# Optimization experiments

Hardware: AMD Instinct MI355X
Metric: run time of the kernel (lower is better)

The kernel has to match this reference:

```python
import jax, jax.numpy as jnp
import numpy as np

B, L, E = 2, 8192, 1024
H, D = 16, 64          # num_heads, head_dim (E = H*D)
C = 256                # chunk_size
EPS = 1e-6
LN_EPS = 1e-5


def setup_inputs() -> dict:
    key = jax.random.key(0)
    ks = jax.random.split(key, 12)
    w = lambda k, shape: (jax.random.normal(k, shape, jnp.float32) * 0.02)
    return {
        "x": jax.random.normal(ks[0], (B, L, E), jnp.float32),
        "Wq": w(ks[1], (E, E)), "bq": jnp.zeros((E,), jnp.float32),
        "Wk": w(ks[2], (E, E)), "bk": jnp.zeros((E,), jnp.float32),
        "Wv": w(ks[3], (E, E)), "bv": jnp.zeros((E,), jnp.float32),
        "Wo": w(ks[4], (E, E)), "bo": jnp.zeros((E,), jnp.float32),
        "gamma": jnp.ones((E,), jnp.float32),
        "beta": jnp.zeros((E,), jnp.float32),
    }


def _split_heads(t):
    # [B, L, E] -> [B, H, L, D]
    return t.reshape(B, L, H, D).transpose(0, 2, 1, 3)


def _phi(x):
    # feature map: elu(x) + 1  (strictly positive)
    return jax.nn.elu(x) + 1.0


def _chunkwise_linear_attention(q, k, v):
    """Causal linear attention via chunkwise parallel scan.

    q, k, v: [B, H, L, D] (q, k already feature-mapped, positive).
    out[t] = q_t @ S_t / (q_t . z_t), S_t = sum_{s<=t} k_s v_s^T, z_t = sum_{s<=t} k_s.
    """
    N = L // C
    # [N, B, H, C, D]
    qc = q.reshape(B, H, N, C, D).transpose(2, 0, 1, 3, 4)
    kc = k.reshape(B, H, N, C, D).transpose(2, 0, 1, 3, 4)
    vc = v.reshape(B, H, N, C, D).transpose(2, 0, 1, 3, 4)
    mask = jnp.tril(jnp.ones((C, C), q.dtype))  # causal within chunk (inclusive)

    def step(carry, inp):
        S, z = carry                      # S: [B,H,D,D], z: [B,H,D]
        qi, ki, vi = inp                  # [B,H,C,D]
        scores = jnp.einsum("bhcd,bhed->bhce", qi, ki) * mask  # [B,H,C,C]
        num = jnp.einsum("bhcd,bhde->bhce", qi, S) \
            + jnp.einsum("bhce,bhed->bhcd", scores, vi)
        den = jnp.einsum("bhcd,bhd->bhc", qi, z) + scores.sum(-1)
        out = num / (den + EPS)[..., None]
        S = S + jnp.einsum("bhcd,bhce->bhde", ki, vi)
        z = z + ki.sum(axis=2)
        return (S, z), out

    S0 = jnp.zeros((B, H, D, D), q.dtype)
    z0 = jnp.zeros((B, H, D), q.dtype)
    _, outs = jax.lax.scan(step, (S0, z0), (qc, kc, vc))
    # [N,B,H,C,D] -> [B,H,L,D]
    return outs.transpose(1, 2, 0, 3, 4).reshape(B, H, L, D)


def _layer_norm(x, gamma, beta):
    mu = x.mean(-1, keepdims=True)
    var = ((x - mu) ** 2).mean(-1, keepdims=True)
    return gamma * (x - mu) * jax.lax.rsqrt(var + LN_EPS) + beta


def reference(x, Wq, bq, Wk, bk, Wv, bv, Wo, bo, gamma, beta):
    residual = x
    q = _phi(_split_heads(x @ Wq + bq))
    k = _phi(_split_heads(x @ Wk + bk))
    v = _split_heads(x @ Wv + bv)
    out = _chunkwise_linear_attention(q, k, v)      # [B,H,L,D]
    out = out.transpose(0, 2, 1, 3).reshape(B, L, E)
    out = out @ Wo + bo
    return _layer_norm(out + residual, gamma, beta)
```

## Files before the change

kernel.cpp:

```cpp
#include <hip/hip_runtime.h>
#include <stdint.h>

typedef __attribute__((ext_vector_type(8))) short bf16x8;
typedef __attribute__((ext_vector_type(4))) float f32x4;
typedef __attribute__((ext_vector_type(2))) unsigned int u32x2;
typedef unsigned short u16;
typedef unsigned int u32;

#define MFMA16(a, b, c) __builtin_amdgcn_mfma_f32_16x16x32_bf16((a), (b), (c), 0, 0, 0)

__device__ __forceinline__ u16 f2bf(float f) {
  union { float f; u32 u; } c; c.f = f;
  u32 u = c.u;
  return (u16)((u + 0x7FFFu + ((u >> 16) & 1u)) >> 16);
}

__device__ __forceinline__ float bf2f(u16 h) {
  union { u32 u; float f; } c;
  c.u = ((u32)h) << 16;
  return c.f;
}

__device__ __forceinline__ void gll16(const void* g, void* l) {
  __builtin_amdgcn_global_load_lds((__attribute__((address_space(1))) void*)(g),
                                   (__attribute__((address_space(3))) void*)(l),
                                   16, 0, 0);
}

__global__ __launch_bounds__(256) void cast_k(const float* __restrict__ x, u16* __restrict__ xb) {
  int idx = blockIdx.x * 256 + threadIdx.x;
#pragma unroll
  for (int it = 0; it < 4; it++) {
    size_t i = (size_t)idx + (size_t)it * 1048576;
    float4 v = ((const float4*)x)[i];
    u32x2 p;
    p.x = (u32)f2bf(v.x) | ((u32)f2bf(v.y) << 16);
    p.y = (u32)f2bf(v.z) | ((u32)f2bf(v.w) << 16);
    ((u32x2*)xb)[i] = p;
  }
}

__global__ __launch_bounds__(256) void wT_k(const float* __restrict__ Wq, const float* __restrict__ Wk,
                                            const float* __restrict__ Wv, const float* __restrict__ Wo,
                                            u16* __restrict__ wqkvT, u16* __restrict__ woT) {
  __shared__ float t[32][33];
  int which = blockIdx.z;
  const float* W = (which == 0) ? Wq : (which == 1) ? Wk : (which == 2) ? Wv : Wo;
  int k0 = blockIdx.y * 32, n0 = blockIdx.x * 32;
  int c = threadIdx.x & 31, r8 = threadIdx.x >> 5;
#pragma unroll
  for (int rr = 0; rr < 32; rr += 8)
    t[r8 + rr][c] = W[(size_t)(k0 + r8 + rr) * 1024 + n0 + c];
  __syncthreads();
  u16* outp = (which < 3) ? (wqkvT + (size_t)which * 1048576) : woT;
#pragma unroll
  for (int rr = 0; rr < 32; rr += 8)
    outp[(size_t)(n0 + r8 + rr) * 1024 + k0 + c] = f2bf(t[c][r8 + rr]);
}

template <int MODE>
__global__ __launch_bounds__(256, 2) void gemm_k(
    const u16* __restrict__ A, const u16* __restrict__ Bt,
    const float* __restrict__ b0, const float* __restrict__ b1, const float* __restrict__ b2,
    u16* __restrict__ q_o, u16* __restrict__ k_o, u16* __restrict__ vt_o,
    const u16* __restrict__ xres, u16* __restrict__ y_o) {
  __shared__ u16 As[2][4096];
  __shared__ u16 Bs[2][4096];
  const int tid = threadIdx.x;
  const int wave = tid >> 6, lane = tid & 63;
  const int quad = lane >> 4, l16 = lane & 15;
  const int wr = wave >> 1, wc = wave & 1;
  const int bm = blockIdx.x, bn = blockIdx.y;

  const int r_a = wave * 32 + (lane >> 2);
  const int c_a = (lane & 3) * 8;
  const size_t arow = (size_t)bm * 128;
  const size_t brow = (size_t)bn * 128;

  f32x4 zero = {0.f, 0.f, 0.f, 0.f};
  f32x4 acc[4][4];
#pragma unroll
  for (int i = 0; i < 4; i++)
#pragma unroll
    for (int j = 0; j < 4; j++) acc[i][j] = zero;

  for (int k0 = 0; k0 < 1024; k0 += 64) {
#pragma unroll
    for (int h = 0; h < 2; h++) {
      const int kk = k0 + h * 32;
#pragma unroll
      for (int jc = 0; jc < 2; jc++) {
        int r = r_a + jc * 16;
        int lo = wave * 1024 + jc * 512 + lane * 8;
        gll16(A + (arow + r) * 1024 + kk + c_a, &As[h][lo]);
        gll16(Bt + (brow + r) * 1024 + kk + c_a, &Bs[h][lo]);
      }
    }
    __syncthreads();
#pragma unroll
    for (int h = 0; h < 2; h++) {
      bf16x8 af[4], bf[4];
#pragma unroll
      for (int t = 0; t < 4; t++) af[t] = *(const bf16x8*)&As[h][(wr * 64 + t * 16 + l16) * 32 + quad * 8];
#pragma unroll
      for (int t = 0; t < 4; t++) bf[t] = *(const bf16x8*)&Bs[h][(wc * 64 + t * 16 + l16) * 32 + quad * 8];
#pragma unroll
      for (int i = 0; i < 4; i++)
#pragma unroll
        for (int j = 0; j < 4; j++) acc[i][j] = MFMA16(af[i], bf[j], acc[i][j]);
    }
    __syncthreads();
  }

  if (MODE == 0) {
#pragma unroll
    for (int i = 0; i < 4; i++) {
      const int m0 = bm * 128 + wr * 64 + i * 16 + quad * 4;
      const int b = m0 >> 13, l0 = m0 & 8191;
      const int nch = l0 >> 8, c0 = l0 & 255;
#pragma unroll
      for (int j = 0; j < 4; j++) {
        const int n_g = bn * 128 + wc * 64 + j * 16 + l16;
        const int sec = n_g >> 10, e = n_g & 1023;
        const float* bias = (sec == 0) ? b0 : ((sec == 1) ? b1 : b2);
        const float be = bias[e];
        float v4[4];
#pragma unroll
        for (int r = 0; r < 4; r++) {
          float v = acc[i][j][r] + be;
          if (sec < 2) v = (v > 0.f) ? (v + 1.f) : __expf(v);
          v4[r] = v;
        }
        const int h = e >> 6, d = e & 63;
        const int bh = b * 16 + h;
        if (sec == 2) {
          u32x2 p;
          p.x = (u32)f2bf(v4[0]) | ((u32)f2bf(v4[1]) << 16);
          p.y = (u32)f2bf(v4[2]) | ((u32)f2bf(v4[3]) << 16);
          *(u32x2*)&vt_o[(((size_t)(bh * 32 + nch)) * 64 + d) * 256 + c0] = p;
        } else {
          u16* dst = (sec == 0) ? q_o : k_o;
          const size_t tb = (((size_t)bh * 8192 + l0) << 6) + d;
#pragma unroll
          for (int r = 0; r < 4; r++) dst[tb + (size_t)r * 64] = f2bf(v4[r]);
        }
      }
    }
  } else {
#pragma unroll
    for (int i = 0; i < 4; i++) {
#pragma unroll
      for (int j = 0; j < 4; j++) {
#pragma unroll
        for (int r = 0; r < 4; r++) {
          int m_g = bm * 128 + wr * 64 + i * 16 + quad * 4 + r;
          int n_g = bn * 128 + wc * 64 + j * 16 + l16;
          float v = acc[i][j][r] + b0[n_g] + bf2f(xres[(size_t)m_g * 1024 + n_g]);
          y_o[(size_t)m_g * 1024 + n_g] = f2bf(v);
        }
      }
    }
  }
}

__global__ __launch_bounds__(256, 2) void phaseA_k(const u16* __restrict__ kb, const u16* __restrict__ vt,
                                                   float* __restrict__ ST, float* __restrict__ zc) {
  __shared__ u16 kT[64 * 264];
  const int tid = threadIdx.x;
  const int wave = tid >> 6, lane = tid & 63;
  const int quad = lane >> 4, l16 = lane & 15;
  const int wr = wave >> 1, wc = wave & 1;
  const int bhn = blockIdx.x;
  const u16* kc = kb + (size_t)bhn * 16384;
  const u16* vtc = vt + (size_t)bhn * 16384;

#pragma unroll
  for (int t = 0; t < 2; t++) {
    const int dblk = wave + 4 * t;
#pragma unroll
    for (int itc = 0; itc < 4; itc++) {
      const int c = itc * 64 + lane;
      bf16x8 kv = *(const bf16x8*)&kc[c * 64 + dblk * 8];
#pragma unroll
      for (int j = 0; j < 8; j++) kT[(dblk * 8 + j) * 264 + c] = (u16)kv[j];
    }
  }
  __syncthreads();

  f32x4 zero = {0.f, 0.f, 0.f, 0.f};
  f32x4 t4[2][2];
  f32x4 za[2];
#pragma unroll
  for (int i = 0; i < 2; i++) {
    za[i] = zero;
#pragma unroll
    for (int j = 0; j < 2; j++) t4[i][j] = zero;
  }
  bf16x8 ones;
#pragma unroll
  for (int j = 0; j < 8; j++) ones[j] = (short)0x3F80;

#pragma unroll
  for (int ks = 0; ks < 8; ks++) {
    bf16x8 av[2], bk2[2];
#pragma unroll
    for (int t = 0; t < 2; t++) av[t] = *(const bf16x8*)&vtc[(wr * 32 + t * 16 + l16) * 256 + ks * 32 + quad * 8];
#pragma unroll
    for (int t = 0; t < 2; t++) bk2[t] = *(const bf16x8*)&kT[(wc * 32 + t * 16 + l16) * 264 + ks * 32 + quad * 8];
#pragma unroll
    for (int i = 0; i < 2; i++)
#pragma unroll
      for (int j = 0; j < 2; j++) t4[i][j] = MFMA16(av[i], bk2[j], t4[i][j]);
    if (wr == 0) {
#pragma unroll
      for (int j = 0; j < 2; j++) za[j] = MFMA16(ones, bk2[j], za[j]);
    }
  }
  float* Sg = ST + (size_t)bhn * 4096;
#pragma unroll
  for (int i = 0; i < 2; i++)
#pragma unroll
    for (int j = 0; j < 2; j++)
#pragma unroll
      for (int r = 0; r < 4; r++)
        Sg[(wr * 32 + i * 16 + quad * 4 + r) * 64 + wc * 32 + j * 16 + l16] = t4[i][j][r];
  if (wr == 0 && quad == 0) {
#pragma unroll
    for (int j = 0; j < 2; j++) zc[(size_t)bhn * 64 + wc * 32 + j * 16 + l16] = za[j][0];
  }
}

__global__ __launch_bounds__(256) void phaseB_k(const float* __restrict__ ST, const float* __restrict__ zc,
                                                u16* __restrict__ STp, u16* __restrict__ zp) {
  const int blk = blockIdx.x, tid = threadIdx.x;
  if (blk < 512) {
    const int bh = blk >> 4;
    const int e = ((blk & 15) << 8) + tid;
    const size_t base = (size_t)bh * 32 * 4096 + e;
    float run = 0.f;
#pragma unroll
    for (int n = 0; n < 32; n++) {
      float v = ST[base + (size_t)n * 4096];
      STp[base + (size_t)n * 4096] = f2bf(run);
      run += v;
    }
  } else {
    const int idx = (blk - 512) * 256 + tid;
    const int bh = idx >> 6, d = idx & 63;
    const size_t zb = (size_t)bh * 2048 + d;
    float run = 0.f;
#pragma unroll
    for (int n = 0; n < 32; n++) {
      float v = zc[zb + n * 64];
      zp[zb + n * 64] = f2bf(run);
      run += v;
    }
  }
}

__global__ __launch_bounds__(256, 2) void phaseC_k(const u16* __restrict__ qb, const u16* __restrict__ kb,
                                                   const u16* __restrict__ vt, const u16* __restrict__ STp,
                                                   const u16* __restrict__ zp, u16* __restrict__ ao) {
  __shared__ u16 P[4][64 * 72];
  const int tid = threadIdx.x;
  const int wave = tid >> 6, lane = tid & 63;
  const int quad = lane >> 4, l16 = lane & 15;
  const int bhn = blockIdx.x;
  const int bh = bhn >> 5, n = bhn & 31;
  const int b = bh >> 4, h = bh & 15;
  const size_t cbase = (size_t)bhn * 16384;
  const u16* qc = qb + cbase;
  const u16* kc = kb + cbase;
  const u16* vtc = vt + cbase;
  const u16* STg = STp + (size_t)bhn * 4096;
  const u16* zg = zp + (size_t)bhn * 64;

  f32x4 zero = {0.f, 0.f, 0.f, 0.f};
  f32x4 num[4][4];
  f32x4 den[4];
#pragma unroll
  for (int i = 0; i < 4; i++) {
    den[i] = zero;
#pragma unroll
    for (int j = 0; j < 4; j++) num[i][j] = zero;
  }
  bf16x8 ones;
#pragma unroll
  for (int j = 0; j < 8; j++) ones[j] = (short)0x3F80;

  bf16x8 aq[4][2];
#pragma unroll
  for (int i = 0; i < 4; i++)
#pragma unroll
    for (int ks = 0; ks < 2; ks++)
      aq[i][ks] = *(const bf16x8*)&qc[(wave * 64 + i * 16 + l16) * 64 + ks * 32 + quad * 8];

#pragma unroll
  for (int ks = 0; ks < 2; ks++) {
    bf16x8 bz = *(const bf16x8*)&zg[ks * 32 + quad * 8];
    bf16x8 bs[4];
#pragma unroll
    for (int j = 0; j < 4; j++) bs[j] = *(const bf16x8*)&STg[(j * 16 + l16) * 64 + ks * 32 + quad * 8];
#pragma unroll
    for (int i = 0; i < 4; i++) {
      den[i] = MFMA16(aq[i][ks], bz, den[i]);
#pragma unroll
      for (int j = 0; j < 4; j++) num[i][j] = MFMA16(aq[i][ks], bs[j], num[i][j]);
    }
  }

  u16* Pw = &P[wave][0];

  for (int cc = 0; cc <= wave; cc++) {
    bf16x8 bkf[2][4];
#pragma unroll
    for (int ks = 0; ks < 2; ks++)
#pragma unroll
      for (int j = 0; j < 4; j++)
        bkf[ks][j] = *(const bf16x8*)&kc[(cc * 64 + j * 16 + l16) * 64 + ks * 32 + quad * 8];
#pragma unroll
    for (int i = 0; i < 4; i++) {
      f32x4 sc4[4];
#pragma unroll
      for (int j = 0; j < 4; j++) sc4[j] = zero;
#pragma unroll
      for (int ks = 0; ks < 2; ks++)
#pragma unroll
        for (int j = 0; j < 4; j++) sc4[j] = MFMA16(aq[i][ks], bkf[ks][j], sc4[j]);
#pragma unroll
      for (int j = 0; j < 4; j++) {
#pragma unroll
        for (int r = 0; r < 4; r++) {
          int row = wave * 64 + i * 16 + quad * 4 + r;
          int col = cc * 64 + j * 16 + l16;
          float v = (col <= row) ? sc4[j][r] : 0.f;
          Pw[(i * 16 + quad * 4 + r) * 72 + j * 16 + l16] = f2bf(v);
        }
      }
    }
    bf16x8 bvf[2][4];
#pragma unroll
    for (int ks2 = 0; ks2 < 2; ks2++)
#pragma unroll
      for (int j = 0; j < 4; j++)
        bvf[ks2][j] = *(const bf16x8*)&vtc[(j * 16 + l16) * 256 + cc * 64 + ks2 * 32 + quad * 8];
#pragma unroll
    for (int i = 0; i < 4; i++) {
#pragma unroll
      for (int ks2 = 0; ks2 < 2; ks2++) {
        bf16x8 ap = *(const bf16x8*)&Pw[(i * 16 + l16) * 72 + ks2 * 32 + quad * 8];
#pragma unroll
        for (int j = 0; j < 4; j++) num[i][j] = MFMA16(ap, bvf[ks2][j], num[i][j]);
        den[i] = MFMA16(ap, ones, den[i]);
      }
    }
  }

#pragma unroll
  for (int i = 0; i < 4; i++)
#pragma unroll
    for (int j = 0; j < 4; j++)
#pragma unroll
      for (int r = 0; r < 4; r++) {
        int row = wave * 64 + i * 16 + quad * 4 + r;
        int col = j * 16 + l16;
        float o = num[i][j][r] / (den[i][r] + 1e-6f);
        int l = n * 256 + row;
        ao[(((size_t)b * 8192 + l) * 16 + h) * 64 + col] = f2bf(o);
      }
}

__global__ __launch_bounds__(256) void ln_k(const u16* __restrict__ y, const float* __restrict__ gamma,
                                            const float* __restrict__ beta, float* __restrict__ o) {
  int row = blockIdx.x, tid = threadIdx.x;
  u32x2 pv = ((const u32x2*)(y + (size_t)row * 1024))[tid];
  float vx = bf2f((u16)(pv.x & 0xFFFF)), vy = bf2f((u16)(pv.x >> 16));
  float vz = bf2f((u16)(pv.y & 0xFFFF)), vw = bf2f((u16)(pv.y >> 16));
  float s = vx + vy + vz + vw;
  float s2 = vx * vx + vy * vy + vz * vz + vw * vw;
#pragma unroll
  for (int off = 32; off; off >>= 1) {
    s += __shfl_down(s, off, 64);
    s2 += __shfl_down(s2, off, 64);
  }
  __shared__ float red[8];
  int wave = tid >> 6, lane = tid & 63;
  if (lane == 0) { red[wave] = s; red[4 + wave] = s2; }
  __syncthreads();
  s = red[0] + red[1] + red[2] + red[3];
  s2 = red[4] + red[5] + red[6] + red[7];
  float mu = s * 0.0009765625f;
  float var = s2 * 0.0009765625f - mu * mu;
  float inv = rsqrtf(var + 1e-5f);
  float4 g = ((const float4*)gamma)[tid];
  float4 bb = ((const float4*)beta)[tid];
  float4 ov;
  ov.x = g.x * (vx - mu) * inv + bb.x;
  ov.y = g.y * (vy - mu) * inv + bb.y;
  ov.z = g.z * (vz - mu) * inv + bb.z;
  ov.w = g.w * (vw - mu) * inv + bb.w;
  ((float4*)(o + (size_t)row * 1024))[tid] = ov;
}

extern "C" void kernel_launch(void* const* d_in, const int* in_sizes, int n_in,
                              void* d_out, int out_size, void* d_ws, size_t ws_size,
                              hipStream_t stream) {
  const float* x = (const float*)d_in[0];
  const float* Wq = (const float*)d_in[1];
  const float* bq = (const float*)d_in[2];
  const float* Wk = (const float*)d_in[3];
  const float* bk = (const float*)d_in[4];
  const float* Wv = (const float*)d_in[5];
  const float* bv = (const float*)d_in[6];
  const float* Wo = (const float*)d_in[7];
  const float* bo = (const float*)d_in[8];
  const float* gamma = (const float*)d_in[9];
  const float* beta = (const float*)d_in[10];

  char* ws = (char*)d_ws;
  u16* xb = (u16*)(ws + 0);
  u16* qb = (u16*)(ws + 33554432);
  u16* kb = (u16*)(ws + 67108864);
  u16* attno = (u16*)(ws + 100663296);
  u16* vt = (u16*)(ws + 134217728);
  u16* wqkvT = (u16*)(ws + 167772160);
  u16* woT = (u16*)(ws + 174063616);
  float* SchT = (float*)(ws + 176160768);
  float* zch = (float*)(ws + 192937984);
  u16* STp = (u16*)(ws + 193200128);
  u16* zp = (u16*)(ws + 201588736);
  u16* ypre = qb;

  cast_k<<<4096, 256, 0, stream>>>(x, xb);
  wT_k<<<dim3(32, 32, 4), 256, 0, stream>>>(Wq, Wk, Wv, Wo, wqkvT, woT);
  gemm_k<0><<<dim3(128, 24), 256, 0, stream>>>(xb, wqkvT, bq, bk, bv, qb, kb, vt, nullptr, nullptr);
  phaseA_k<<<1024, 256, 0, stream>>>(kb, vt, SchT, zch);
  phaseB_k<<<520, 256, 0, stream>>>(SchT, zch, STp, zp);
  phaseC_k<<<1024, 256, 0, stream>>>(qb, kb, vt, STp, zp, attno);
  gemm_k<1><<<dim3(128, 8), 256, 0, stream>>>(attno, woT, bo, nullptr, nullptr, nullptr, nullptr, nullptr, xb,
                                              ypre);
  ln_k<<<16384, 256, 0, stream>>>(ypre, gamma, beta, (float*)d_out);
}
```

Baseline: 388.8 us.

## Rewrite projection GEMMs as 256x256 tiles with swizzled LDS and interleaved prefetch

Both projection GEMMs go from 128x128 tiles with 256 threads to 256x256 tiles with 512 threads and 8 waves. K steps are 64 wide, LDS layouts are XOR-swizzled, and global-to-LDS loads for the next step are issued in quarters between MFMA groups, using explicit vmcnt waits, raw barriers and setprio. The goal is more data reuse per tile, fewer LDS bank conflicts, and load latency hidden behind compute. In exchange, LDS use is 128 KB per block, so occupancy is likely one block per CU. The grid also shrinks (768 and 256 blocks), which may underfill the 256 CUs, especially for the output GEMM.

New measurement: 371.3 us. -4.5%, faster.

```diff
diff --git a/kernel.cpp b/kernel.cpp
--- a/kernel.cpp
+++ b/kernel.cpp
@@ -8,6 +8,8 @@
 typedef unsigned int u32;
 
 #define MFMA16(a, b, c) __builtin_amdgcn_mfma_f32_16x16x32_bf16((a), (b), (c), 0, 0, 0)
+#define SBAR() asm volatile("s_barrier" ::: "memory")
+#define WAITV(N) asm volatile("s_waitcnt vmcnt(" #N ")" ::: "memory")
 
 __device__ __forceinline__ u16 f2bf(float f) {
   union { float f; u32 u; } c; c.f = f;
@@ -58,69 +60,158 @@
     outp[(size_t)(n0 + r8 + rr) * 1024 + k0 + c] = f2bf(t[c][r8 + rr]);
 }
 
+__device__ __forceinline__ void stage_half(const u16* g, u16* l, int tid) {
+  gll16(g, l + tid * 8);
+  gll16(g + 65536, l + 4096 + tid * 8);
+}
+
+__device__ __forceinline__ bf16x8 fragld(const u16* h, int r, int slot) {
+  return *(const bf16x8*)(h + r * 64 + ((slot ^ (r & 7)) << 3));
+}
+
 template <int MODE>
-__global__ __launch_bounds__(256, 2) void gemm_k(
+__global__ __launch_bounds__(512, 2) void gemm_k(
     const u16* __restrict__ A, const u16* __restrict__ Bt,
     const float* __restrict__ b0, const float* __restrict__ b1, const float* __restrict__ b2,
     u16* __restrict__ q_o, u16* __restrict__ k_o, u16* __restrict__ vt_o,
     const u16* __restrict__ xres, u16* __restrict__ y_o) {
-  __shared__ u16 As[2][4096];
-  __shared__ u16 Bs[2][4096];
+  __shared__ u16 As[2][2][8192];
+  __shared__ u16 Bs[2][2][8192];
   const int tid = threadIdx.x;
   const int wave = tid >> 6, lane = tid & 63;
   const int quad = lane >> 4, l16 = lane & 15;
-  const int wr = wave >> 1, wc = wave & 1;
+  const int wr = wave >> 2, wc = wave & 3;
   const int bm = blockIdx.x, bn = blockIdx.y;
-
-  const int r_a = wave * 32 + (lane >> 2);
-  const int c_a = (lane & 3) * 8;
-  const size_t arow = (size_t)bm * 128;
-  const size_t brow = (size_t)bn * 128;
+  const size_t arow = (size_t)bm * 256;
+  const size_t brow = (size_t)bn * 256;
+
+  const int r0 = tid >> 3;
+  const int s8 = tid & 7;
+  const int swz = (s8 ^ (r0 & 7)) << 3;
+  const u16* gA = A + (arow + r0) * 1024 + swz;
+  const u16* gB = Bt + (brow + r0) * 1024 + swz;
 
   f32x4 zero = {0.f, 0.f, 0.f, 0.f};
-  f32x4 acc[4][4];
-#pragma unroll
-  for (int i = 0; i < 4; i++)
+  f32x4 acc[8][4];
+#pragma unroll
+  for (int i = 0; i < 8; i++)
 #pragma unroll
     for (int j = 0; j < 4; j++) acc[i][j] = zero;
 
-  for (int k0 = 0; k0 < 1024; k0 += 64) {
-#pragma unroll
-    for (int h = 0; h < 2; h++) {
-      const int kk = k0 + h * 32;
-#pragma unroll
-      for (int jc = 0; jc < 2; jc++) {
-        int r = r_a + jc * 16;
-        int lo = wave * 1024 + jc * 512 + lane * 8;
-        gll16(A + (arow + r) * 1024 + kk + c_a, &As[h][lo]);
-        gll16(Bt + (brow + r) * 1024 + kk + c_a, &Bs[h][lo]);
+  stage_half(gA, &As[0][0][0], tid);
+  stage_half(gA + 131072, &As[0][1][0], tid);
+  stage_half(gB, &Bs[0][0][0], tid);
+  stage_half(gB + 131072, &Bs[0][1][0], tid);
+  stage_half(gB + 64, &Bs[1][0][0], tid);
+  stage_half(gB + 131072 + 64, &Bs[1][1][0], tid);
+  WAITV(4);
+  SBAR();
+
+  const int bno = (wc & 1) * 64;
+#pragma unroll 2
+  for (int t = 0; t < 16; ++t) {
+    const int cb = t & 1, nb = cb ^ 1;
+    const u16* Ah = &As[cb][wr][0];
+    const u16* Bh = &Bs[cb][wc >> 1][0];
+
+    bf16x8 bfr[4][2];
+#pragma unroll
+    for (int n = 0; n < 4; n++)
+#pragma unroll
+      for (int ks = 0; ks < 2; ks++)
+        bfr[n][ks] = fragld(Bh, bno + n * 16 + l16, ks * 4 + quad);
+    {
+      bf16x8 am[2][2];
+#pragma unroll
+      for (int m = 0; m < 2; m++)
+#pragma unroll
+        for (int ks = 0; ks < 2; ks++)
+          am[m][ks] = fragld(Ah, m * 16 + l16, ks * 4 + quad);
+      if (t < 15) stage_half(gA + (t + 1) * 64, &As[nb][0][0], tid);
+      SBAR();
+      __builtin_amdgcn_s_setprio(1);
+#pragma unroll
+      for (int ks = 0; ks < 2; ks++)
+#pragma unroll
+        for (int m = 0; m < 2; m++)
+#pragma unroll
+          for (int n = 0; n < 4; n++) acc[m][n] = MFMA16(am[m][ks], bfr[n][ks], acc[m][n]);
+      __builtin_amdgcn_s_setprio(0);
+      SBAR();
+    }
+    {
+      bf16x8 am[2][2];
+#pragma unroll
+      for (int m = 0; m < 2; m++)
+#pragma unroll
+        for (int ks = 0; ks < 2; ks++)
+          am[m][ks] = fragld(Ah, 32 + m * 16 + l16, ks * 4 + quad);
+      if (t < 15) stage_half(gA + 131072 + (t + 1) * 64, &As[nb][1][0], tid);
+      SBAR();
+      __builtin_amdgcn_s_setprio(1);
+#pragma unroll
+      for (int ks = 0; ks < 2; ks++)
+#pragma unroll
+        for (int m = 0; m < 2; m++)
+#pragma unroll
+          for (int n = 0; n < 4; n++) acc[2 + m][n] = MFMA16(am[m][ks], bfr[n][ks], acc[2 + m][n]);
+      __builtin_amdgcn_s_setprio(0);
+      SBAR();
+    }
+    {
+      bf16x8 am[2][2];
+#pragma unroll
+      for (int m = 0; m < 2; m++)
+#pragma unroll
+        for (int ks = 0; ks < 2; ks++)
+          am[m][ks] = fragld(Ah, 64 + m * 16 + l16, ks * 4 + quad);
+      if (t < 14) stage_half(gB + (t + 2) * 64, &Bs[cb][0][0], tid);
+      SBAR();
+      __builtin_amdgcn_s_setprio(1);
+#pragma unroll
+      for (int ks = 0; ks < 2; ks++)
+#pragma unroll
+        for (int m = 0; m < 2; m++)
+#pragma unroll
+          for (int n = 0; n < 4; n++) acc[4 + m][n] = MFMA16(am[m][ks], bfr[n][ks], acc[4 + m][n]);
+      __builtin_amdgcn_s_setprio(0);
+      SBAR();
+    }
+    {
+      bf16x8 am[2][2];
+#pragma unroll
+      for (int m = 0; m < 2; m++)
+#pragma unroll
+        for (int ks = 0; ks < 2; ks++)
+          am[m][ks] = fragld(Ah, 96 + m * 16 + l16, ks * 4 + quad);
+      if (t < 14) stage_half(gB + 131072 + (t + 2) * 64, &Bs[cb][1][0], tid);
+      SBAR();
+      __builtin_amdgcn_s_setprio(1);
+#pragma unroll
+      for (int ks = 0; ks < 2; ks++)
+#pragma unroll
+        for (int m = 0; m < 2; m++)
+#pragma unroll
+          for (int n = 0; n < 4; n++) acc[6 + m][n] = MFMA16(am[m][ks], bfr[n][ks], acc[6 + m][n]);
+      __builtin_amdgcn_s_setprio(0);
+      if (t < 14) {
+        WAITV(4);
+      } else if (t == 14) {
+        WAITV(0);
       }
-    }
-    __syncthreads();
-#pragma unroll
-    for (int h = 0; h < 2; h++) {
-      bf16x8 af[4], bf[4];
-#pragma unroll
-      for (int t = 0; t < 4; t++) af[t] = *(const bf16x8*)&As[h][(wr * 64 + t * 16 + l16) * 32 + quad * 8];
-#pragma unroll
-      for (int t = 0; t < 4; t++) bf[t] = *(const bf16x8*)&Bs[h][(wc * 64 + t * 16 + l16) * 32 + quad * 8];
-#pragma unroll
-      for (int i = 0; i < 4; i++)
-#pragma unroll
-        for (int j = 0; j < 4; j++) acc[i][j] = MFMA16(af[i], bf[j], acc[i][j]);
-    }
-    __syncthreads();
+      SBAR();
+    }
   }
 
   if (MODE == 0) {
 #pragma unroll
-    for (int i = 0; i < 4; i++) {
-      const int m0 = bm * 128 + wr * 64 + i * 16 + quad * 4;
+    for (int i = 0; i < 8; i++) {
+      const int m0 = bm * 256 + wr * 128 + i * 16 + quad * 4;
       const int b = m0 >> 13, l0 = m0 & 8191;
       const int nch = l0 >> 8, c0 = l0 & 255;
 #pragma unroll
       for (int j = 0; j < 4; j++) {
-        const int n_g = bn * 128 + wc * 64 + j * 16 + l16;
+        const int n_g = bn * 256 + wc * 64 + j * 16 + l16;
         const int sec = n_g >> 10, e = n_g & 1023;
         const float* bias = (sec == 0) ? b0 : ((sec == 1) ? b1 : b2);
         const float be = bias[e];
@@ -148,13 +239,13 @@
     }
   } else {
 #pragma unroll
-    for (int i = 0; i < 4; i++) {
+    for (int i = 0; i < 8; i++) {
 #pragma unroll
       for (int j = 0; j < 4; j++) {
 #pragma unroll
         for (int r = 0; r < 4; r++) {
-          int m_g = bm * 128 + wr * 64 + i * 16 + quad * 4 + r;
-          int n_g = bn * 128 + wc * 64 + j * 16 + l16;
+          int m_g = bm * 256 + wr * 128 + i * 16 + quad * 4 + r;
+          int n_g = bn * 256 + wc * 64 + j * 16 + l16;
           float v = acc[i][j][r] + b0[n_g] + bf2f(xres[(size_t)m_g * 1024 + n_g]);
           y_o[(size_t)m_g * 1024 + n_g] = f2bf(v);
         }
@@ -433,11 +524,11 @@
 
   cast_k<<<4096, 256, 0, stream>>>(x, xb);
   wT_k<<<dim3(32, 32, 4), 256, 0, stream>>>(Wq, Wk, Wv, Wo, wqkvT, woT);
-  gemm_k<0><<<dim3(128, 24), 256, 0, stream>>>(xb, wqkvT, bq, bk, bv, qb, kb, vt, nullptr, nullptr);
+  gemm_k<0><<<dim3(64, 12), 512, 0, stream>>>(xb, wqkvT, bq, bk, bv, qb, kb, vt, nullptr, nullptr);
   phaseA_k<<<1024, 256, 0, stream>>>(kb, vt, SchT, zch);
   phaseB_k<<<520, 256, 0, stream>>>(SchT, zch, STp, zp);
   phaseC_k<<<1024, 256, 0, stream>>>(qb, kb, vt, STp, zp, attno);
-  gemm_k<1><<<dim3(128, 8), 256, 0, stream>>>(attno, woT, bo, nullptr, nullptr, nullptr, nullptr, nullptr, xb,
-                                              ypre);
+  gemm_k<1><<<dim3(64, 4), 512, 0, stream>>>(attno, woT, bo, nullptr, nullptr, nullptr, nullptr, nullptr, xb,
+                                             ypre);
   ln_k<<<16384, 256, 0, stream>>>(ypre, gamma, beta, (float*)d_out);
 }
```
